# Performance work log

Measured on AMD Instinct MI355X. Metric: run time of the kernel, lower is better.

Reference implementation:

```python
import jax, jax.numpy as jnp
import numpy as np

N = 50000        # nodes
E = 800000       # edges (before self loops)
IN = 128         # in_channels
HID = 32         # hidden_channels (per head)
HEADS = 4
OUT = 10         # out_channels (classes)
G = 64           # graphs in batch
NEG_SLOPE = 0.2  # PyG GATConv default leaky relu slope


def setup_inputs() -> dict:
    key = jax.random.key(0)
    ks = jax.random.split(key, 12)
    s = 0.05
    return {
        "x": jax.random.normal(ks[0], (N, IN), jnp.float32),
        "W1": jax.random.normal(ks[1], (IN, HEADS * HID), jnp.float32) * s,
        "a1_src": jax.random.normal(ks[2], (HEADS, HID), jnp.float32) * s,
        "a1_dst": jax.random.normal(ks[3], (HEADS, HID), jnp.float32) * s,
        "b1": jnp.zeros((HEADS * HID,), jnp.float32),
        "W2": jax.random.normal(ks[4], (HEADS * HID, HEADS * HID), jnp.float32) * s,
        "a2_src": jax.random.normal(ks[5], (HEADS, HID), jnp.float32) * s,
        "a2_dst": jax.random.normal(ks[6], (HEADS, HID), jnp.float32) * s,
        "b2": jnp.zeros((HEADS * HID,), jnp.float32),
        "Wl": jax.random.normal(ks[7], (HEADS * HID, OUT), jnp.float32) * s,
        "bl": jnp.zeros((OUT,), jnp.float32),
        "edge_index": jax.random.randint(ks[8], (2, E), 0, N, jnp.int32),
        "batch": jnp.sort(jax.random.randint(ks[9], (N,), 0, G, jnp.int32)),
    }


def gat_conv(x, src, dst, W, a_src, a_dst, b):
    """PyG GATConv (concat=True, self loops already in src/dst). Eval mode: no dropout."""
    n = x.shape[0]
    h = (x @ W).reshape(n, HEADS, HID)                       # [N,H,C]
    al_s = jnp.einsum('nhc,hc->nh', h, a_src)                # [N,H]
    al_d = jnp.einsum('nhc,hc->nh', h, a_dst)
    e = jax.nn.leaky_relu(al_s[src] + al_d[dst], NEG_SLOPE)  # [Etot,H]
    # segment softmax over destination node neighborhoods
    m = jax.ops.segment_max(e, dst, num_segments=n)
    m = jnp.where(jnp.isfinite(m), m, 0.0)
    p = jnp.exp(e - m[dst])
    z = jax.ops.segment_sum(p, dst, num_segments=n)
    alpha = p / (z[dst] + 1e-16)                             # [Etot,H]
    out = jax.ops.segment_sum(h[src] * alpha[:, :, None], dst, num_segments=n)
    return out.reshape(n, HEADS * HID) + b


def reference(x, W1, a1_src, a1_dst, b1, W2, a2_src, a2_dst, b2, Wl, bl,
              edge_index, batch):
    n = x.shape[0]
    loops = jnp.arange(n, dtype=edge_index.dtype)
    src = jnp.concatenate([edge_index[0], loops])
    dst = jnp.concatenate([edge_index[1], loops])

    h = jax.nn.elu(gat_conv(x, src, dst, W1, a1_src, a1_dst, b1))
    h = gat_conv(h, src, dst, W2, a2_src, a2_dst, b2)

    # global_mean_pool over graph ids
    counts = jax.ops.segment_sum(jnp.ones((n,), h.dtype), batch, num_segments=G)
    pooled = jax.ops.segment_sum(h, batch, num_segments=G) / jnp.maximum(counts, 1.0)[:, None]

    logits = pooled @ Wl + bl
    return jax.nn.softmax(logits, axis=1)
```

## Files before the change

kernel.cpp:

```cpp
#include <hip/hip_runtime.h>
#include <hip/hip_bf16.h>
#include <math.h>

#define HEADS 4
#define HID 32
#define FDIM 128
#define OUTC 10
#define NEG 0.2f
#define ECAP 512
#define BCAP 5440

typedef __attribute__((ext_vector_type(4))) float f32x4;
typedef __attribute__((ext_vector_type(8))) short bf16x8;

static __device__ __forceinline__ float lrelu(float v) { return v > 0.f ? v : NEG * v; }

static __device__ __forceinline__ unsigned bfr(float f) {
  unsigned u = __float_as_uint(f);
  return (u + 0x7fffu + ((u >> 16) & 1u)) >> 16;
}
static __device__ __forceinline__ float blo(unsigned u) { return __uint_as_float(u << 16); }
static __device__ __forceinline__ float bhi(unsigned u) { return __uint_as_float(u & 0xffff0000u); }

#define CHUNK 4096

__global__ __launch_bounds__(256) void k_bin(
    const int* __restrict__ ei, int* __restrict__ gbcur,
    int2* __restrict__ bbuf, int E, int n) {
  __shared__ int h[256];
  __shared__ int cur[256];
  int tid = threadIdx.x;
  h[tid] = 0;
  __syncthreads();
  int base = blockIdx.x * CHUNK;
  int tot = E + n;
  #pragma unroll
  for (int r = 0; r < 16; ++r) {
    int e = base + r * 256 + tid;
    if (e < tot) {
      int dst = (e < E) ? ei[E + e] : (e - E);
      atomicAdd(&h[dst >> 8], 1);
    }
  }
  __syncthreads();
  if (h[tid]) cur[tid] = tid * BCAP + atomicAdd(&gbcur[tid], h[tid]);
  __syncthreads();
  #pragma unroll
  for (int r = 0; r < 16; ++r) {
    int e = base + r * 256 + tid;
    if (e < tot) {
      int src = (e < E) ? ei[e] : (e - E);
      int dst = (e < E) ? ei[E + e] : (e - E);
      int pos = atomicAdd(&cur[dst >> 8], 1);
      bbuf[pos] = make_int2(src, dst);
    }
  }
}

__global__ __launch_bounds__(256) void k_build(
    const int2* __restrict__ bbuf, const int* __restrict__ gbcur,
    int* __restrict__ offs, int* __restrict__ csr, int* __restrict__ dpos,
    int n) {
  __shared__ int deg[256];
  __shared__ int sc[256];
  __shared__ int cur[256];
  int b = blockIdx.x;
  int tid = threadIdx.x;
  int ebeg = b * BCAP;
  int eend = ebeg + gbcur[b];
  deg[tid] = 0;
  __syncthreads();
  for (int i = ebeg + tid; i < eend; i += 256)
    atomicAdd(&deg[bbuf[i].y & 255], 1);
  __syncthreads();
  int v = deg[tid];
  sc[tid] = v;
  __syncthreads();
  #pragma unroll
  for (int off = 1; off < 256; off <<= 1) {
    int t = (tid >= off) ? sc[tid - off] : 0;
    __syncthreads();
    sc[tid] += t;
    __syncthreads();
  }
  int excl = sc[tid] - v;
  int dst0 = b * 256 + tid;
  if (dst0 < n) offs[dst0] = ebeg + excl;
  cur[tid] = ebeg + excl;
  __syncthreads();
  for (int i = ebeg + tid; i < eend; i += 256) {
    int2 sd = bbuf[i];
    int pos = atomicAdd(&cur[sd.y & 255], 1);
    csr[pos] = sd.x;
    dpos[pos] = sd.y;
  }
}

__global__ __launch_bounds__(256) void k_prep(
    const float* __restrict__ W1, const float* __restrict__ W2,
    const float* __restrict__ a1s, const float* __restrict__ a1d,
    const float* __restrict__ a2s, const float* __restrict__ a2d,
    uint4* __restrict__ WF) {
  int layer = blockIdx.y;
  const float* W = layer ? W2 : W1;
  __shared__ float wa[128][8];
  int tid = threadIdx.x;
  #pragma unroll
  for (int q = 0; q < 4; ++q) {
    int e = tid * 4 + q;
    int k = e >> 3, c = e & 7;
    int h = c & 3;
    const float* av = (c < 4 ? (layer ? a2s : a1s) : (layer ? a2d : a1d)) + h * 32;
    const float* wr = W + (size_t)k * 128 + h * 32;
    float s = 0.f;
    #pragma unroll
    for (int j = 0; j < 32; j += 4) {
      float4 wv = *reinterpret_cast<const float4*>(wr + j);
      float4 a4 = *reinterpret_cast<const float4*>(av + j);
      s += wv.x * a4.x + wv.y * a4.y + wv.z * a4.z + wv.w * a4.w;
    }
    wa[k][c] = s;
  }
  __syncthreads();
  int gid = blockIdx.x * 256 + tid;
  if (gid >= 2304) return;
  int lane = gid & 63, frag = gid >> 6;
  int t = frag / 9, ct = frag - t * 9;
  int quad = lane >> 4, r = lane & 15;
  int kbase = t * 32 + quad * 8;
  unsigned v[8];
  if (ct < 8) {
    int col = ct * 16 + r;
    #pragma unroll
    for (int j = 0; j < 8; ++j) v[j] = bfr(W[(size_t)(kbase + j) * 128 + col]);
  } else if (r < 8) {
    #pragma unroll
    for (int j = 0; j < 8; ++j) v[j] = bfr(wa[kbase + j][r]);
  } else {
    #pragma unroll
    for (int j = 0; j < 8; ++j) v[j] = 0;
  }
  uint4 pk;
  pk.x = v[0] | (v[1] << 16);
  pk.y = v[2] | (v[3] << 16);
  pk.z = v[4] | (v[5] << 16);
  pk.w = v[6] | (v[7] << 16);
  WF[layer * 2304 + gid] = pk;
}

template<bool BF16IN>
__global__ __launch_bounds__(256) void k_mm(
    const void* __restrict__ Xv, const uint4* __restrict__ WF,
    unsigned short* __restrict__ H, float* __restrict__ AL, int n) {
  __shared__ uint4 wf[2304];
  int tid = threadIdx.x;
  #pragma unroll
  for (int i = 0; i < 9; ++i) wf[i * 256 + tid] = WF[i * 256 + tid];
  __syncthreads();
  int lane = tid & 63, wid = tid >> 6;
  int quad = lane >> 4, r = lane & 15;
  int rowbase = blockIdx.x * 64 + wid * 16;
  int arow = rowbase + r;
  int arowc = arow < n ? arow : 0;
  const bf16x8* wfs = (const bf16x8*)wf;

  f32x4 acc[9];
  #pragma unroll
  for (int ct = 0; ct < 9; ++ct) acc[ct] = 0;

  #pragma unroll
  for (int t = 0; t < 4; ++t) {
    bf16x8 a;
    if (BF16IN) {
      const uint4* xp = reinterpret_cast<const uint4*>(Xv) + (size_t)arowc * 16;
      uint4 u = xp[t * 4 + quad];
      a = *reinterpret_cast<const bf16x8*>(&u);
    } else {
      const float* xp = reinterpret_cast<const float*>(Xv) + (size_t)arowc * 128 + quad * 8;
      float4 x0 = *reinterpret_cast<const float4*>(xp + t * 32);
      float4 x1 = *reinterpret_cast<const float4*>(xp + t * 32 + 4);
      a[0] = (short)bfr(x0.x); a[1] = (short)bfr(x0.y);
      a[2] = (short)bfr(x0.z); a[3] = (short)bfr(x0.w);
      a[4] = (short)bfr(x1.x); a[5] = (short)bfr(x1.y);
      a[6] = (short)bfr(x1.z); a[7] = (short)bfr(x1.w);
    }
    #pragma unroll
    for (int ct = 0; ct < 9; ++ct)
      acc[ct] = __builtin_amdgcn_mfma_f32_16x16x32_bf16(
          a, wfs[(t * 9 + ct) * 64 + lane], acc[ct], 0, 0, 0);
  }

  int orow0 = rowbase + quad * 4;
  #pragma unroll
  for (int rr = 0; rr < 4; ++rr) {
    int orow = orow0 + rr;
    if (orow < n) {
      unsigned short* hp = H + (size_t)orow * 128 + r;
      #pragma unroll
      for (int ct = 0; ct < 8; ++ct) hp[ct * 16] = (unsigned short)bfr(acc[ct][rr]);
      if (r < 8) AL[(size_t)orow * 8 + r] = acc[8][rr];
    }
  }
}

template<bool ELU_OUT, bool POOL>
__global__ __launch_bounds__(256) void k_agg(
    const unsigned short* __restrict__ H, const float* __restrict__ AL,
    const int* __restrict__ offs, const int* __restrict__ csr,
    const int* __restrict__ dpos, const int* __restrict__ gbcur,
    const float* __restrict__ bias, unsigned short* __restrict__ OUT,
    const int* __restrict__ batch, float* __restrict__ pooled,
    int* __restrict__ gcnt, int n) {
  __shared__ __align__(16) char smem[ECAP * 4 + ECAP * 16];
  int* s_l = (int*)smem;
  float (*p_l)[4] = (float(*)[4])(smem + ECAP * 4);
  float (*o_l)[132] = (float(*)[132])smem;
  __shared__ int g_l[16];
  int tid = threadIdx.x;
  int lane = tid & 63;
  int r = lane & 15;
  int gg = (tid >> 6) * 4 + (lane >> 4);
  int nbase = blockIdx.x * 16;
  int node = nbase + gg;
  bool nvalid = node < n;
  int nodec = nvalid ? node : 0;
  int bkt = nbase >> 8;
  int bend = bkt * BCAP + gbcur[bkt];
  int beg = offs[nodec];
  int nxt = nodec + 1;
  int end = nvalid ? ((nxt >= n || (nxt & 255) == 0) ? bend : offs[nxt]) : beg;
  int ebeg = offs[nbase];
  int nend = nbase + 16;
  int eend = (nend >= n || (nend & 255) == 0) ? bend : offs[nend];
  int hsel = r >> 2;
  const uint4* hb = reinterpret_cast<const uint4*>(H) + r;

  if (POOL && r == 0) g_l[gg] = nvalid ? batch[node] : -1;

  float z = 0.f;
  float acc[8];
  #pragma unroll
  for (int k = 0; k < 8; ++k) acc[k] = 0.f;

  for (int c0 = ebeg; c0 < eend; c0 += ECAP) {
    int clen = min(ECAP, eend - c0);
    __syncthreads();
    for (int i = tid; i < clen; i += 256) {
      int s = csr[c0 + i];
      int d = dpos[c0 + i];
      float4 as_ = *reinterpret_cast<const float4*>(AL + (size_t)s * 8);
      float4 ad = *reinterpret_cast<const float4*>(AL + (size_t)d * 8 + 4);
      s_l[i] = s;
      float4 p;
      p.x = __expf(lrelu(as_.x + ad.x));
      p.y = __expf(lrelu(as_.y + ad.y));
      p.z = __expf(lrelu(as_.z + ad.z));
      p.w = __expf(lrelu(as_.w + ad.w));
      *reinterpret_cast<float4*>(&p_l[i][0]) = p;
    }
    __syncthreads();
    int lo = max(beg, c0), hi = min(end, c0 + clen);
    int cnt = hi - lo;
    int lbase = lo - c0;
    for (int j0 = 0; j0 < cnt; j0 += 4) {
      int j1 = j0 + 1, j2 = j0 + 2, j3 = j0 + 3;
      bool v1 = j1 < cnt, v2 = j2 < cnt, v3 = j3 < cnt;
      int jB = lbase + (v1 ? j1 : j0);
      int jC = lbase + (v2 ? j2 : j0);
      int jD = lbase + (v3 ? j3 : j0);
      int jA = lbase + j0;
      int sA = s_l[jA], sB = s_l[jB], sC = s_l[jC], sD = s_l[jD];
      float pA = p_l[jA][hsel];
      float pB = v1 ? p_l[jB][hsel] : 0.f;
      float pC = v2 ? p_l[jC][hsel] : 0.f;
      float pD = v3 ? p_l[jD][hsel] : 0.f;
      z += (pA + pB) + (pC + pD);
      uint4 uA = hb[(size_t)sA * 16];
      uint4 uB = hb[(size_t)sB * 16];
      uint4 uC = hb[(size_t)sC * 16];
      uint4 uD = hb[(size_t)sD * 16];
      acc[0] = fmaf(pA, blo(uA.x), acc[0]); acc[1] = fmaf(pA, bhi(uA.x), acc[1]);
      acc[2] = fmaf(pA, blo(uA.y), acc[2]); acc[3] = fmaf(pA, bhi(uA.y), acc[3]);
      acc[4] = fmaf(pA, blo(uA.z), acc[4]); acc[5] = fmaf(pA, bhi(uA.z), acc[5]);
      acc[6] = fmaf(pA, blo(uA.w), acc[6]); acc[7] = fmaf(pA, bhi(uA.w), acc[7]);
      acc[0] = fmaf(pB, blo(uB.x), acc[0]); acc[1] = fmaf(pB, bhi(uB.x), acc[1]);
      acc[2] = fmaf(pB, blo(uB.y), acc[2]); acc[3] = fmaf(pB, bhi(uB.y), acc[3]);
      acc[4] = fmaf(pB, blo(uB.z), acc[4]); acc[5] = fmaf(pB, bhi(uB.z), acc[5]);
      acc[6] = fmaf(pB, blo(uB.w), acc[6]); acc[7] = fmaf(pB, bhi(uB.w), acc[7]);
      acc[0] = fmaf(pC, blo(uC.x), acc[0]); acc[1] = fmaf(pC, bhi(uC.x), acc[1]);
      acc[2] = fmaf(pC, blo(uC.y), acc[2]); acc[3] = fmaf(pC, bhi(uC.y), acc[3]);
      acc[4] = fmaf(pC, blo(uC.z), acc[4]); acc[5] = fmaf(pC, bhi(uC.z), acc[5]);
      acc[6] = fmaf(pC, blo(uC.w), acc[6]); acc[7] = fmaf(pC, bhi(uC.w), acc[7]);
      acc[0] = fmaf(pD, blo(uD.x), acc[0]); acc[1] = fmaf(pD, bhi(uD.x), acc[1]);
      acc[2] = fmaf(pD, blo(uD.y), acc[2]); acc[3] = fmaf(pD, bhi(uD.y), acc[3]);
      acc[4] = fmaf(pD, blo(uD.z), acc[4]); acc[5] = fmaf(pD, bhi(uD.z), acc[5]);
      acc[6] = fmaf(pD, blo(uD.w), acc[6]); acc[7] = fmaf(pD, bhi(uD.w), acc[7]);
    }
  }

  float inv = 1.f / (z + 1e-16f);
  int f0 = r * 8;
  float4 b0 = *reinterpret_cast<const float4*>(bias + f0);
  float4 b1 = *reinterpret_cast<const float4*>(bias + f0 + 4);
  float o[8];
  o[0] = acc[0] * inv + b0.x; o[1] = acc[1] * inv + b0.y;
  o[2] = acc[2] * inv + b0.z; o[3] = acc[3] * inv + b0.w;
  o[4] = acc[4] * inv + b1.x; o[5] = acc[5] * inv + b1.y;
  o[6] = acc[6] * inv + b1.z; o[7] = acc[7] * inv + b1.w;
  if (ELU_OUT) {
    #pragma unroll
    for (int k = 0; k < 8; ++k) o[k] = o[k] > 0.f ? o[k] : expm1f(o[k]);
  }

  if (!POOL) {
    if (nvalid) {
      uint4 pk;
      pk.x = bfr(o[0]) | (bfr(o[1]) << 16);
      pk.y = bfr(o[2]) | (bfr(o[3]) << 16);
      pk.z = bfr(o[4]) | (bfr(o[5]) << 16);
      pk.w = bfr(o[6]) | (bfr(o[7]) << 16);
      reinterpret_cast<uint4*>(OUT)[(size_t)node * 16 + r] = pk;
    }
  } else {
    __syncthreads();
    *reinterpret_cast<float4*>(&o_l[gg][f0]) = make_float4(o[0], o[1], o[2], o[3]);
    *reinterpret_cast<float4*>(&o_l[gg][f0 + 4]) = make_float4(o[4], o[5], o[6], o[7]);
    __syncthreads();
    if (tid < 128) {
      int f = tid;
      float accp = 0.f; int cur = -1;
      #pragma unroll
      for (int i = 0; i < 16; ++i) {
        int g = g_l[i];
        if (g != cur) {
          if (cur >= 0) atomicAdd(&pooled[(size_t)cur * 128 + f], accp);
          cur = g; accp = 0.f;
        }
        if (g >= 0) accp += o_l[i][f];
      }
      if (cur >= 0) atomicAdd(&pooled[(size_t)cur * 128 + f], accp);
    } else if (tid == 128) {
      int cur = -1, c = 0;
      #pragma unroll
      for (int i = 0; i < 16; ++i) {
        int g = g_l[i];
        if (g != cur) { if (cur >= 0) atomicAdd(&gcnt[cur], c); cur = g; c = 0; }
        if (g >= 0) ++c;
      }
      if (cur >= 0) atomicAdd(&gcnt[cur], c);
    }
  }
}

__global__ void k_head(const float* __restrict__ pooled, const int* __restrict__ gcnt,
                       const float* __restrict__ Wl, const float* __restrict__ bl,
                       float* __restrict__ out) {
  int g = blockIdx.x;
  int lane = threadIdx.x;
  float cnt = fmaxf((float)gcnt[g], 1.f);
  float pA = pooled[(size_t)g * 128 + lane] / cnt;
  float pB = pooled[(size_t)g * 128 + lane + 64] / cnt;
  float l[OUTC];
  #pragma unroll
  for (int o = 0; o < OUTC; ++o) {
    float s = pA * Wl[lane * OUTC + o] + pB * Wl[(lane + 64) * OUTC + o];
    #pragma unroll
    for (int off = 32; off; off >>= 1) s += __shfl_xor(s, off);
    l[o] = s + bl[o];
  }
  float mx = l[0];
  #pragma unroll
  for (int o = 1; o < OUTC; ++o) mx = fmaxf(mx, l[o]);
  float se = 0.f;
  #pragma unroll
  for (int o = 0; o < OUTC; ++o) { l[o] = __expf(l[o] - mx); se += l[o]; }
  if (lane == 0) {
    float inv = 1.f / se;
    #pragma unroll
    for (int o = 0; o < OUTC; ++o) out[g * OUTC + o] = l[o] * inv;
  }
}

extern "C" void kernel_launch(void* const* d_in, const int* in_sizes, int n_in,
                              void* d_out, int out_size, void* d_ws, size_t ws_size,
                              hipStream_t stream) {
  const float* x   = (const float*)d_in[0];
  const float* W1  = (const float*)d_in[1];
  const float* a1s = (const float*)d_in[2];
  const float* a1d = (const float*)d_in[3];
  const float* b1  = (const float*)d_in[4];
  const float* W2  = (const float*)d_in[5];
  const float* a2s = (const float*)d_in[6];
  const float* a2d = (const float*)d_in[7];
  const float* b2  = (const float*)d_in[8];
  const float* Wl  = (const float*)d_in[9];
  const float* bl  = (const float*)d_in[10];
  const int* ei    = (const int*)d_in[11];
  const int* batch = (const int*)d_in[12];
  const int N = in_sizes[12];
  const int E = in_sizes[11] / 2;
  const int G = out_size / OUTC;
  float* out = (float*)d_out;
  (void)n_in; (void)ws_size;

  const int tot = E + N;
  const int NB = (N + 255) / 256;

  char* w = (char*)d_ws;
  auto alloc = [&](size_t bytes) { char* p = w; w += (bytes + 255) & ~(size_t)255; return (void*)p; };
  unsigned short* H = (unsigned short*)alloc((size_t)N * FDIM * sizeof(unsigned short));
  unsigned short* ACT = (unsigned short*)alloc((size_t)N * FDIM * sizeof(unsigned short));
  float* AL     = (float*)alloc((size_t)N * 8 * sizeof(float));
  uint4* WF     = (uint4*)alloc(2 * 2304 * sizeof(uint4));
  int*   offs   = (int*)alloc((size_t)N * sizeof(int));
  int*   csr    = (int*)alloc((size_t)NB * BCAP * sizeof(int));
  int*   dpos   = (int*)alloc((size_t)NB * BCAP * sizeof(int));
  int2*  bbuf   = (int2*)alloc((size_t)NB * BCAP * sizeof(int2));
  char* z0 = w;
  int*   gbcur  = (int*)alloc(256 * sizeof(int));
  int*   gcnt   = (int*)alloc((size_t)G * sizeof(int));
  float* pooled = (float*)alloc((size_t)G * FDIM * sizeof(float));
  size_t zbytes = (size_t)(w - z0);
  hipMemsetAsync(z0, 0, zbytes, stream);

  int ab4 = (tot + CHUNK - 1) / CHUNK;
  k_bin<<<ab4, 256, 0, stream>>>(ei, gbcur, bbuf, E, N);
  k_build<<<NB, 256, 0, stream>>>(bbuf, gbcur, offs, csr, dpos, N);

  k_prep<<<dim3(9, 2), 256, 0, stream>>>(W1, W2, a1s, a1d, a2s, a2d, WF);

  int gb = (N + 63) / 64;
  int ab = (N + 15) / 16;
  k_mm<false><<<gb, 256, 0, stream>>>(x, WF, H, AL, N);
  k_agg<true, false><<<ab, 256, 0, stream>>>(H, AL, offs, csr, dpos, gbcur, b1, ACT, batch, pooled, gcnt, N);
  k_mm<true><<<gb, 256, 0, stream>>>(ACT, WF + 2304, H, AL, N);
  k_agg<false, true><<<ab, 256, 0, stream>>>(H, AL, offs, csr, dpos, gbcur, b2, nullptr, batch, pooled, gcnt, N);

  k_head<<<G, 64, 0, stream>>>(pooled, gcnt, Wl, bl, out);
}
```

Baseline: 230.9 us.

## Compute attention weights per lane with software-prefetched CSR, drop dpos and LDS staging

The aggregation kernel no longer stages source indices and per-edge exp weights in shared memory behind block barriers. Each 16-lane group now reads its node's CSR neighbours directly, computes the leaky-relu exp for its own head, and prefetches the next four neighbour indices and source logits while processing the current four. The dpos array and its writes in the CSR build are removed, since the destination logit is loaded once per node. This trades the shared-memory staging and barriers for redundant exp work across lanes of the same head and more dependent global loads per edge.

```diff
diff --git a/kernel.cpp b/kernel.cpp
--- a/kernel.cpp
+++ b/kernel.cpp
@@ -7,7 +7,6 @@
 #define FDIM 128
 #define OUTC 10
 #define NEG 0.2f
-#define ECAP 512
 #define BCAP 5440
 
 typedef __attribute__((ext_vector_type(4))) float f32x4;
@@ -59,8 +58,7 @@
 
 __global__ __launch_bounds__(256) void k_build(
     const int2* __restrict__ bbuf, const int* __restrict__ gbcur,
-    int* __restrict__ offs, int* __restrict__ csr, int* __restrict__ dpos,
-    int n) {
+    int* __restrict__ offs, int* __restrict__ csr, int n) {
   __shared__ int deg[256];
   __shared__ int sc[256];
   __shared__ int cur[256];
@@ -92,7 +90,6 @@
     int2 sd = bbuf[i];
     int pos = atomicAdd(&cur[sd.y & 255], 1);
     csr[pos] = sd.x;
-    dpos[pos] = sd.y;
   }
 }
 
@@ -207,15 +204,10 @@
 __global__ __launch_bounds__(256) void k_agg(
     const unsigned short* __restrict__ H, const float* __restrict__ AL,
     const int* __restrict__ offs, const int* __restrict__ csr,
-    const int* __restrict__ dpos, const int* __restrict__ gbcur,
+    const int* __restrict__ gbcur,
     const float* __restrict__ bias, unsigned short* __restrict__ OUT,
     const int* __restrict__ batch, float* __restrict__ pooled,
     int* __restrict__ gcnt, int n) {
-  __shared__ __align__(16) char smem[ECAP * 4 + ECAP * 16];
-  int* s_l = (int*)smem;
-  float (*p_l)[4] = (float(*)[4])(smem + ECAP * 4);
-  float (*o_l)[132] = (float(*)[132])smem;
-  __shared__ int g_l[16];
   int tid = threadIdx.x;
   int lane = tid & 63;
   int r = lane & 15;
@@ -229,73 +221,66 @@
   int beg = offs[nodec];
   int nxt = nodec + 1;
   int end = nvalid ? ((nxt >= n || (nxt & 255) == 0) ? bend : offs[nxt]) : beg;
-  int ebeg = offs[nbase];
-  int nend = nbase + 16;
-  int eend = (nend >= n || (nend & 255) == 0) ? bend : offs[nend];
   int hsel = r >> 2;
   const uint4* hb = reinterpret_cast<const uint4*>(H) + r;
-
-  if (POOL && r == 0) g_l[gg] = nvalid ? batch[node] : -1;
+  const float* ALh = AL + hsel;
+  float adv = AL[(size_t)nodec * 8 + 4 + hsel];
 
   float z = 0.f;
   float acc[8];
   #pragma unroll
   for (int k = 0; k < 8; ++k) acc[k] = 0.f;
 
-  for (int c0 = ebeg; c0 < eend; c0 += ECAP) {
-    int clen = min(ECAP, eend - c0);
-    __syncthreads();
-    for (int i = tid; i < clen; i += 256) {
-      int s = csr[c0 + i];
-      int d = dpos[c0 + i];
-      float4 as_ = *reinterpret_cast<const float4*>(AL + (size_t)s * 8);
-      float4 ad = *reinterpret_cast<const float4*>(AL + (size_t)d * 8 + 4);
-      s_l[i] = s;
-      float4 p;
-      p.x = __expf(lrelu(as_.x + ad.x));
-      p.y = __expf(lrelu(as_.y + ad.y));
-      p.z = __expf(lrelu(as_.z + ad.z));
-      p.w = __expf(lrelu(as_.w + ad.w));
-      *reinterpret_cast<float4*>(&p_l[i][0]) = p;
-    }
-    __syncthreads();
-    int lo = max(beg, c0), hi = min(end, c0 + clen);
-    int cnt = hi - lo;
-    int lbase = lo - c0;
-    for (int j0 = 0; j0 < cnt; j0 += 4) {
-      int j1 = j0 + 1, j2 = j0 + 2, j3 = j0 + 3;
-      bool v1 = j1 < cnt, v2 = j2 < cnt, v3 = j3 < cnt;
-      int jB = lbase + (v1 ? j1 : j0);
-      int jC = lbase + (v2 ? j2 : j0);
-      int jD = lbase + (v3 ? j3 : j0);
-      int jA = lbase + j0;
-      int sA = s_l[jA], sB = s_l[jB], sC = s_l[jC], sD = s_l[jD];
-      float pA = p_l[jA][hsel];
-      float pB = v1 ? p_l[jB][hsel] : 0.f;
-      float pC = v2 ? p_l[jC][hsel] : 0.f;
-      float pD = v3 ? p_l[jD][hsel] : 0.f;
-      z += (pA + pB) + (pC + pD);
-      uint4 uA = hb[(size_t)sA * 16];
-      uint4 uB = hb[(size_t)sB * 16];
-      uint4 uC = hb[(size_t)sC * 16];
-      uint4 uD = hb[(size_t)sD * 16];
-      acc[0] = fmaf(pA, blo(uA.x), acc[0]); acc[1] = fmaf(pA, bhi(uA.x), acc[1]);
-      acc[2] = fmaf(pA, blo(uA.y), acc[2]); acc[3] = fmaf(pA, bhi(uA.y), acc[3]);
-      acc[4] = fmaf(pA, blo(uA.z), acc[4]); acc[5] = fmaf(pA, bhi(uA.z), acc[5]);
-      acc[6] = fmaf(pA, blo(uA.w), acc[6]); acc[7] = fmaf(pA, bhi(uA.w), acc[7]);
-      acc[0] = fmaf(pB, blo(uB.x), acc[0]); acc[1] = fmaf(pB, bhi(uB.x), acc[1]);
-      acc[2] = fmaf(pB, blo(uB.y), acc[2]); acc[3] = fmaf(pB, bhi(uB.y), acc[3]);
-      acc[4] = fmaf(pB, blo(uB.z), acc[4]); acc[5] = fmaf(pB, bhi(uB.z), acc[5]);
-      acc[6] = fmaf(pB, blo(uB.w), acc[6]); acc[7] = fmaf(pB, bhi(uB.w), acc[7]);
-      acc[0] = fmaf(pC, blo(uC.x), acc[0]); acc[1] = fmaf(pC, bhi(uC.x), acc[1]);
-      acc[2] = fmaf(pC, blo(uC.y), acc[2]); acc[3] = fmaf(pC, bhi(uC.y), acc[3]);
-      acc[4] = fmaf(pC, blo(uC.z), acc[4]); acc[5] = fmaf(pC, bhi(uC.z), acc[5]);
-      acc[6] = fmaf(pC, blo(uC.w), acc[6]); acc[7] = fmaf(pC, bhi(uC.w), acc[7]);
-      acc[0] = fmaf(pD, blo(uD.x), acc[0]); acc[1] = fmaf(pD, bhi(uD.x), acc[1]);
-      acc[2] = fmaf(pD, blo(uD.y), acc[2]); acc[3] = fmaf(pD, bhi(uD.y), acc[3]);
-      acc[4] = fmaf(pD, blo(uD.z), acc[4]); acc[5] = fmaf(pD, bhi(uD.z), acc[5]);
-      acc[6] = fmaf(pD, blo(uD.w), acc[6]); acc[7] = fmaf(pD, bhi(uD.w), acc[7]);
-    }
+  int cnt = end - beg;
+  int mlast = cnt > 1 ? cnt - 1 : 0;
+
+  int sA = csr[beg + min(0, mlast)];
+  int sB = csr[beg + min(1, mlast)];
+  int sC = csr[beg + min(2, mlast)];
+  int sD = csr[beg + min(3, mlast)];
+  float aA = ALh[(size_t)sA * 8];
+  float aB = ALh[(size_t)sB * 8];
+  float aC = ALh[(size_t)sC * 8];
+  float aD = ALh[(size_t)sD * 8];
+
+  for (int j0 = 0; j0 < cnt; j0 += 4) {
+    uint4 uA = hb[(size_t)sA * 16];
+    uint4 uB = hb[(size_t)sB * 16];
+    uint4 uC = hb[(size_t)sC * 16];
+    uint4 uD = hb[(size_t)sD * 16];
+    int nj = j0 + 4;
+    int tA = csr[beg + min(nj, mlast)];
+    int tB = csr[beg + min(nj + 1, mlast)];
+    int tC = csr[beg + min(nj + 2, mlast)];
+    int tD = csr[beg + min(nj + 3, mlast)];
+    float bA = ALh[(size_t)tA * 8];
+    float bB = ALh[(size_t)tB * 8];
+    float bC = ALh[(size_t)tC * 8];
+    float bD = ALh[(size_t)tD * 8];
+    bool v1 = j0 + 1 < cnt, v2 = j0 + 2 < cnt, v3 = j0 + 3 < cnt;
+    float pA = __expf(lrelu(aA + adv));
+    float pB = v1 ? __expf(lrelu(aB + adv)) : 0.f;
+    float pC = v2 ? __expf(lrelu(aC + adv)) : 0.f;
+    float pD = v3 ? __expf(lrelu(aD + adv)) : 0.f;
+    z += (pA + pB) + (pC + pD);
+    acc[0] = fmaf(pA, blo(uA.x), acc[0]); acc[1] = fmaf(pA, bhi(uA.x), acc[1]);
+    acc[2] = fmaf(pA, blo(uA.y), acc[2]); acc[3] = fmaf(pA, bhi(uA.y), acc[3]);
+    acc[4] = fmaf(pA, blo(uA.z), acc[4]); acc[5] = fmaf(pA, bhi(uA.z), acc[5]);
+    acc[6] = fmaf(pA, blo(uA.w), acc[6]); acc[7] = fmaf(pA, bhi(uA.w), acc[7]);
+    acc[0] = fmaf(pB, blo(uB.x), acc[0]); acc[1] = fmaf(pB, bhi(uB.x), acc[1]);
+    acc[2] = fmaf(pB, blo(uB.y), acc[2]); acc[3] = fmaf(pB, bhi(uB.y), acc[3]);
+    acc[4] = fmaf(pB, blo(uB.z), acc[4]); acc[5] = fmaf(pB, bhi(uB.z), acc[5]);
+    acc[6] = fmaf(pB, blo(uB.w), acc[6]); acc[7] = fmaf(pB, bhi(uB.w), acc[7]);
+    acc[0] = fmaf(pC, blo(uC.x), acc[0]); acc[1] = fmaf(pC, bhi(uC.x), acc[1]);
+    acc[2] = fmaf(pC, blo(uC.y), acc[2]); acc[3] = fmaf(pC, bhi(uC.y), acc[3]);
+    acc[4] = fmaf(pC, blo(uC.z), acc[4]); acc[5] = fmaf(pC, bhi(uC.z), acc[5]);
+    acc[6] = fmaf(pC, blo(uC.w), acc[6]); acc[7] = fmaf(pC, bhi(uC.w), acc[7]);
+    acc[0] = fmaf(pD, blo(uD.x), acc[0]); acc[1] = fmaf(pD, bhi(uD.x), acc[1]);
+    acc[2] = fmaf(pD, blo(uD.y), acc[2]); acc[3] = fmaf(pD, bhi(uD.y), acc[3]);
+    acc[4] = fmaf(pD, blo(uD.z), acc[4]); acc[5] = fmaf(pD, bhi(uD.z), acc[5]);
+    acc[6] = fmaf(pD, blo(uD.w), acc[6]); acc[7] = fmaf(pD, bhi(uD.w), acc[7]);
+    sA = tA; sB = tB; sC = tC; sD = tD;
+    aA = bA; aB = bB; aC = bC; aD = bD;
   }
 
   float inv = 1.f / (z + 1e-16f);
@@ -322,7 +307,9 @@
       reinterpret_cast<uint4*>(OUT)[(size_t)node * 16 + r] = pk;
     }
   } else {
-    __syncthreads();
+    __shared__ __align__(16) float o_l[16][132];
+    __shared__ int g_l[16];
+    if (r == 0) g_l[gg] = nvalid ? batch[node] : -1;
     *reinterpret_cast<float4*>(&o_l[gg][f0]) = make_float4(o[0], o[1], o[2], o[3]);
     *reinterpret_cast<float4*>(&o_l[gg][f0 + 4]) = make_float4(o[4], o[5], o[6], o[7]);
     __syncthreads();
@@ -414,7 +401,6 @@
   uint4* WF     = (uint4*)alloc(2 * 2304 * sizeof(uint4));
   int*   offs   = (int*)alloc((size_t)N * sizeof(int));
   int*   csr    = (int*)alloc((size_t)NB * BCAP * sizeof(int));
-  int*   dpos   = (int*)alloc((size_t)NB * BCAP * sizeof(int));
   int2*  bbuf   = (int2*)alloc((size_t)NB * BCAP * sizeof(int2));
   char* z0 = w;
   int*   gbcur  = (int*)alloc(256 * sizeof(int));
@@ -425,16 +411,16 @@
 
   int ab4 = (tot + CHUNK - 1) / CHUNK;
   k_bin<<<ab4, 256, 0, stream>>>(ei, gbcur, bbuf, E, N);
-  k_build<<<NB, 256, 0, stream>>>(bbuf, gbcur, offs, csr, dpos, N);
+  k_build<<<NB, 256, 0, stream>>>(bbuf, gbcur, offs, csr, N);
 
   k_prep<<<dim3(9, 2), 256, 0, stream>>>(W1, W2, a1s, a1d, a2s, a2d, WF);
 
   int gb = (N + 63) / 64;
   int ab = (N + 15) / 16;
   k_mm<false><<<gb, 256, 0, stream>>>(x, WF, H, AL, N);
-  k_agg<true, false><<<ab, 256, 0, stream>>>(H, AL, offs, csr, dpos, gbcur, b1, ACT, batch, pooled, gcnt, N);
+  k_agg<true, false><<<ab, 256, 0, stream>>>(H, AL, offs, csr, gbcur, b1, ACT, batch, pooled, gcnt, N);
   k_mm<true><<<gb, 256, 0, stream>>>(ACT, WF + 2304, H, AL, N);
-  k_agg<false, true><<<ab, 256, 0, stream>>>(H, AL, offs, csr, dpos, gbcur, b2, nullptr, batch, pooled, gcnt, N);
+  k_agg<false, true><<<ab, 256, 0, stream>>>(H, AL, offs, csr, gbcur, b2, nullptr, batch, pooled, gcnt, N);
 
   k_head<<<G, 64, 0, stream>>>(pooled, gcnt, Wl, bl, out);
 }
```

Result: slower. 239.2 us (+3.6%).

## Make edge-score staging per-wavefront and drop the dpos array

Applied to the files above, without the earlier changes.

Each wavefront now stages the edges of its own four destination nodes into a private shared-memory slice, which removes the block-wide __syncthreads around every chunk. The destination attention term is loaded once per node into registers and picked by comparing the edge index against node boundaries, so the dpos array is no longer written in k_build or read in k_agg. This reduces global traffic and block-level stalls. The risks are wavefront-local LDS ordering relying on an explicit waitcnt, and smaller chunks for high-degree nodes.

```diff
diff --git a/kernel.cpp b/kernel.cpp
--- a/kernel.cpp
+++ b/kernel.cpp
@@ -7,7 +7,7 @@
 #define FDIM 128
 #define OUTC 10
 #define NEG 0.2f
-#define ECAP 512
+#define WCAP 192
 #define BCAP 5440
 
 typedef __attribute__((ext_vector_type(4))) float f32x4;
@@ -59,8 +59,7 @@
 
 __global__ __launch_bounds__(256) void k_build(
     const int2* __restrict__ bbuf, const int* __restrict__ gbcur,
-    int* __restrict__ offs, int* __restrict__ csr, int* __restrict__ dpos,
-    int n) {
+    int* __restrict__ offs, int* __restrict__ csr, int n) {
   __shared__ int deg[256];
   __shared__ int sc[256];
   __shared__ int cur[256];
@@ -92,7 +91,6 @@
     int2 sd = bbuf[i];
     int pos = atomicAdd(&cur[sd.y & 255], 1);
     csr[pos] = sd.x;
-    dpos[pos] = sd.y;
   }
 }
 
@@ -207,33 +205,45 @@
 __global__ __launch_bounds__(256) void k_agg(
     const unsigned short* __restrict__ H, const float* __restrict__ AL,
     const int* __restrict__ offs, const int* __restrict__ csr,
-    const int* __restrict__ dpos, const int* __restrict__ gbcur,
+    const int* __restrict__ gbcur,
     const float* __restrict__ bias, unsigned short* __restrict__ OUT,
     const int* __restrict__ batch, float* __restrict__ pooled,
     int* __restrict__ gcnt, int n) {
-  __shared__ __align__(16) char smem[ECAP * 4 + ECAP * 16];
+  __shared__ __align__(16) char smem[4 * WCAP * 20];
   int* s_l = (int*)smem;
-  float (*p_l)[4] = (float(*)[4])(smem + ECAP * 4);
+  float (*p_l)[4] = (float(*)[4])(smem + 4 * WCAP * 4);
   float (*o_l)[132] = (float(*)[132])smem;
   __shared__ int g_l[16];
   int tid = threadIdx.x;
   int lane = tid & 63;
+  int wid = tid >> 6;
   int r = lane & 15;
-  int gg = (tid >> 6) * 4 + (lane >> 4);
+  int g = lane >> 4;
+  int gg = wid * 4 + g;
   int nbase = blockIdx.x * 16;
   int node = nbase + gg;
   bool nvalid = node < n;
-  int nodec = nvalid ? node : 0;
   int bkt = nbase >> 8;
   int bend = bkt * BCAP + gbcur[bkt];
-  int beg = offs[nodec];
-  int nxt = nodec + 1;
-  int end = nvalid ? ((nxt >= n || (nxt & 255) == 0) ? bend : offs[nxt]) : beg;
-  int ebeg = offs[nbase];
-  int nend = nbase + 16;
-  int eend = (nend >= n || (nend & 255) == 0) ? bend : offs[nend];
+
+  int wn0 = nbase + wid * 4;
+  int wbeg = (wn0 < n) ? offs[wn0] : bend;
+  int b1 = (wn0 + 1 < n) ? offs[wn0 + 1] : bend;
+  int b2 = (wn0 + 2 < n) ? offs[wn0 + 2] : bend;
+  int b3 = (wn0 + 3 < n) ? offs[wn0 + 3] : bend;
+  int wend = (wn0 + 4 >= n || ((wn0 + 4) & 255) == 0) ? bend : offs[wn0 + 4];
+
+  int beg = nvalid ? offs[node] : 0;
+  int end = nvalid ? ((node + 1 >= n || ((node + 1) & 255) == 0) ? bend : offs[node + 1]) : 0;
+
+  float4 ad0 = *reinterpret_cast<const float4*>(AL + (size_t)min(wn0 + 0, n - 1) * 8 + 4);
+  float4 ad1 = *reinterpret_cast<const float4*>(AL + (size_t)min(wn0 + 1, n - 1) * 8 + 4);
+  float4 ad2 = *reinterpret_cast<const float4*>(AL + (size_t)min(wn0 + 2, n - 1) * 8 + 4);
+  float4 ad3 = *reinterpret_cast<const float4*>(AL + (size_t)min(wn0 + 3, n - 1) * 8 + 4);
+
   int hsel = r >> 2;
   const uint4* hb = reinterpret_cast<const uint4*>(H) + r;
+  int sbase = wid * WCAP;
 
   if (POOL && r == 0) g_l[gg] = nvalid ? batch[node] : -1;
 
@@ -242,26 +252,27 @@
   #pragma unroll
   for (int k = 0; k < 8; ++k) acc[k] = 0.f;
 
-  for (int c0 = ebeg; c0 < eend; c0 += ECAP) {
-    int clen = min(ECAP, eend - c0);
-    __syncthreads();
-    for (int i = tid; i < clen; i += 256) {
-      int s = csr[c0 + i];
-      int d = dpos[c0 + i];
+  for (int c0 = wbeg; c0 < wend; c0 += WCAP) {
+    int clen = min(WCAP, wend - c0);
+    for (int i = lane; i < clen; i += 64) {
+      int e = c0 + i;
+      int s = csr[e];
       float4 as_ = *reinterpret_cast<const float4*>(AL + (size_t)s * 8);
-      float4 ad = *reinterpret_cast<const float4*>(AL + (size_t)d * 8 + 4);
-      s_l[i] = s;
+      int idx = (e >= b1) + (e >= b2) + (e >= b3);
+      float4 ad = idx == 0 ? ad0 : (idx == 1 ? ad1 : (idx == 2 ? ad2 : ad3));
+      s_l[sbase + i] = s;
       float4 p;
       p.x = __expf(lrelu(as_.x + ad.x));
       p.y = __expf(lrelu(as_.y + ad.y));
       p.z = __expf(lrelu(as_.z + ad.z));
       p.w = __expf(lrelu(as_.w + ad.w));
-      *reinterpret_cast<float4*>(&p_l[i][0]) = p;
-    }
-    __syncthreads();
+      *reinterpret_cast<float4*>(&p_l[sbase + i][0]) = p;
+    }
+    asm volatile("s_waitcnt lgkmcnt(0)" ::: "memory");
+    __builtin_amdgcn_sched_barrier(0);
     int lo = max(beg, c0), hi = min(end, c0 + clen);
     int cnt = hi - lo;
-    int lbase = lo - c0;
+    int lbase = sbase + (lo - c0);
     for (int j0 = 0; j0 < cnt; j0 += 4) {
       int j1 = j0 + 1, j2 = j0 + 2, j3 = j0 + 3;
       bool v1 = j1 < cnt, v2 = j2 < cnt, v3 = j3 < cnt;
@@ -301,12 +312,12 @@
   float inv = 1.f / (z + 1e-16f);
   int f0 = r * 8;
   float4 b0 = *reinterpret_cast<const float4*>(bias + f0);
-  float4 b1 = *reinterpret_cast<const float4*>(bias + f0 + 4);
+  float4 b1v = *reinterpret_cast<const float4*>(bias + f0 + 4);
   float o[8];
   o[0] = acc[0] * inv + b0.x; o[1] = acc[1] * inv + b0.y;
   o[2] = acc[2] * inv + b0.z; o[3] = acc[3] * inv + b0.w;
-  o[4] = acc[4] * inv + b1.x; o[5] = acc[5] * inv + b1.y;
-  o[6] = acc[6] * inv + b1.z; o[7] = acc[7] * inv + b1.w;
+  o[4] = acc[4] * inv + b1v.x; o[5] = acc[5] * inv + b1v.y;
+  o[6] = acc[6] * inv + b1v.z; o[7] = acc[7] * inv + b1v.w;
   if (ELU_OUT) {
     #pragma unroll
     for (int k = 0; k < 8; ++k) o[k] = o[k] > 0.f ? o[k] : expm1f(o[k]);
@@ -331,21 +342,21 @@
       float accp = 0.f; int cur = -1;
       #pragma unroll
       for (int i = 0; i < 16; ++i) {
-        int g = g_l[i];
-        if (g != cur) {
+        int gq = g_l[i];
+        if (gq != cur) {
           if (cur >= 0) atomicAdd(&pooled[(size_t)cur * 128 + f], accp);
-          cur = g; accp = 0.f;
+          cur = gq; accp = 0.f;
         }
-        if (g >= 0) accp += o_l[i][f];
+        if (gq >= 0) accp += o_l[i][f];
       }
       if (cur >= 0) atomicAdd(&pooled[(size_t)cur * 128 + f], accp);
     } else if (tid == 128) {
       int cur = -1, c = 0;
       #pragma unroll
       for (int i = 0; i < 16; ++i) {
-        int g = g_l[i];
-        if (g != cur) { if (cur >= 0) atomicAdd(&gcnt[cur], c); cur = g; c = 0; }
-        if (g >= 0) ++c;
+        int gq = g_l[i];
+        if (gq != cur) { if (cur >= 0) atomicAdd(&gcnt[cur], c); cur = gq; c = 0; }
+        if (gq >= 0) ++c;
       }
       if (cur >= 0) atomicAdd(&gcnt[cur], c);
     }
@@ -414,7 +425,6 @@
   uint4* WF     = (uint4*)alloc(2 * 2304 * sizeof(uint4));
   int*   offs   = (int*)alloc((size_t)N * sizeof(int));
   int*   csr    = (int*)alloc((size_t)NB * BCAP * sizeof(int));
-  int*   dpos   = (int*)alloc((size_t)NB * BCAP * sizeof(int));
   int2*  bbuf   = (int2*)alloc((size_t)NB * BCAP * sizeof(int2));
   char* z0 = w;
   int*   gbcur  = (int*)alloc(256 * sizeof(int));
@@ -425,16 +435,16 @@
 
   int ab4 = (tot + CHUNK - 1) / CHUNK;
   k_bin<<<ab4, 256, 0, stream>>>(ei, gbcur, bbuf, E, N);
-  k_build<<<NB, 256, 0, stream>>>(bbuf, gbcur, offs, csr, dpos, N);
+  k_build<<<NB, 256, 0, stream>>>(bbuf, gbcur, offs, csr, N);
 
   k_prep<<<dim3(9, 2), 256, 0, stream>>>(W1, W2, a1s, a1d, a2s, a2d, WF);
 
   int gb = (N + 63) / 64;
   int ab = (N + 15) / 16;
   k_mm<false><<<gb, 256, 0, stream>>>(x, WF, H, AL, N);
-  k_agg<true, false><<<ab, 256, 0, stream>>>(H, AL, offs, csr, dpos, gbcur, b1, ACT, batch, pooled, gcnt, N);
+  k_agg<true, false><<<ab, 256, 0, stream>>>(H, AL, offs, csr, gbcur, b1, ACT, batch, pooled, gcnt, N);
   k_mm<true><<<gb, 256, 0, stream>>>(ACT, WF + 2304, H, AL, N);
-  k_agg<false, true><<<ab, 256, 0, stream>>>(H, AL, offs, csr, dpos, gbcur, b2, nullptr, batch, pooled, gcnt, N);
+  k_agg<false, true><<<ab, 256, 0, stream>>>(H, AL, offs, csr, gbcur, b2, nullptr, batch, pooled, gcnt, N);
 
   k_head<<<G, 64, 0, stream>>>(pooled, gcnt, Wl, bl, out);
 }
```

New measurement: 236.3 us. +2.3%, slower.
